# Kernel optimization log

Hardware: AMD Instinct MI355X
Metric: run time of the kernel (lower is better)

Reference implementation:

```python
import jax, jax.numpy as jnp
import numpy as np

N_FFT = 4096
HOP = 1024
WIN = 300          # wiener_win_len (frames per independent Wiener chunk)
EPS = 1e-10
SCALE_FACTOR = 10.0


def hann(n):
    # torch.hann_window (periodic)
    return 0.5 * (1.0 - jnp.cos(2.0 * jnp.pi * jnp.arange(n) / n))


def stft(x, window):
    # x: (N, C, T) -> complex (N, C, B, F), center=True, reflect pad, onesided
    pad = N_FFT // 2
    xp = jnp.pad(x, ((0, 0), (0, 0), (pad, pad)), mode='reflect')
    n_frames = 1 + (xp.shape[-1] - N_FFT) // HOP
    idx = jnp.arange(n_frames)[:, None] * HOP + jnp.arange(N_FFT)[None, :]
    frames = xp[..., idx] * window                      # (N,C,F,n_fft)
    spec = jnp.fft.rfft(frames, axis=-1)                # (N,C,F,B)
    return jnp.swapaxes(spec, -1, -2)                   # (N,C,B,F)


def istft(spec, window, length):
    # spec: (..., B, F) complex -> (..., length) real; center=True inverse
    frames = jnp.fft.irfft(jnp.swapaxes(spec, -1, -2), n=N_FFT, axis=-1) * window
    n_frames = frames.shape[-2]
    out_len = N_FFT + HOP * (n_frames - 1)
    idx = jnp.arange(n_frames)[:, None] * HOP + jnp.arange(N_FFT)[None, :]
    out = jnp.zeros(frames.shape[:-2] + (out_len,), frames.dtype).at[..., idx].add(frames)
    wsum = jnp.zeros((out_len,), frames.dtype).at[idx].add(
        jnp.broadcast_to(window ** 2, idx.shape))
    out = out / jnp.where(wsum > 1e-11, wsum, 1.0)
    pad = N_FFT // 2
    return out[..., pad:pad + length]


def wiener_chunk(v, x, niter):
    # openunmix.filtering.wiener (softmask=False, residual=False) on one chunk.
    # v: (T, B, C, S) real target magnitudes; x: (T, B, C) complex mix STFT.
    phase = jnp.exp(1j * jnp.angle(x))                  # mixture phase init
    y = (v * phase[..., None]).astype(jnp.complex64)    # (T,B,C,S)
    max_abs = jnp.maximum(1.0, jnp.max(jnp.abs(x)) / SCALE_FACTOR)
    x = x / max_abs
    y = y / max_abs
    C = x.shape[-1]
    reg = np.sqrt(EPS) * jnp.eye(C, dtype=jnp.complex64)
    for _ in range(niter):  # expectation_maximization, one pass per iter
        psd = jnp.mean(jnp.abs(y) ** 2, axis=2)         # (T,B,S) channel-avg PSD
        # spatial covariance per bin/source, normalized by eps + sum_t psd
        R = jnp.einsum('tbcs,tbds->bcds', y, jnp.conj(y))
        R = R / (EPS + jnp.sum(psd, axis=0))[:, None, None, :]
        Cxx = reg + jnp.einsum('tbs,bcds->tbcd', psd.astype(jnp.complex64), R)
        inv = jnp.linalg.inv(Cxx)                       # (T,B,C,C)
        gain = jnp.einsum('bacs,tbcd->tbads', R, inv) * psd[:, :, None, None, :]
        y = jnp.einsum('tbacs,tbc->tbas', gain, x)      # (T,B,C,S)
    return y * max_abs


def setup_inputs() -> dict:
    key = jax.random.key(0)
    k1, k2 = jax.random.split(key)
    audio = jax.random.normal(k1, (2, 2, 613376), dtype=jnp.float32)
    W = jax.random.normal(k2, (4, 2049), dtype=jnp.float32)  # per-target per-bin mask logits
    return {'audio': audio, 'W': W, 'niter': 1}


def reference(audio, W, niter):
    window = hann(N_FFT).astype(audio.dtype)
    mix = stft(audio, window)                           # (N,C,B,F) complex
    X = jnp.abs(mix)                                    # ComplexNorm power=1
    # target models (stand-in: per-bin sigmoid masks); input detached as in torch
    Xd = jax.lax.stop_gradient(X)
    masks = jax.nn.sigmoid(W)                           # (S,B)
    specs = Xd[..., None] * jnp.transpose(masks)[None, None, :, None, :]  # (N,C,B,F,S)
    v = jnp.transpose(specs, (0, 3, 2, 1, 4))           # (N,F,B,C,S)
    xm = jnp.transpose(mix, (0, 3, 2, 1))               # (N,F,B,C)
    N, F, B, C = xm.shape
    S = v.shape[-1]
    n_chunks = F // WIN
    vc = v.reshape(N, n_chunks, WIN, B, C, S)
    xc = xm.reshape(N, n_chunks, WIN, B, C)
    wfun = lambda vv, xx: wiener_chunk(vv, xx, niter)
    yc = jax.vmap(jax.vmap(wfun))(vc, xc)               # (N,chunks,T,B,C,S)
    y = yc.reshape(N, F, B, C, S)
    y = jnp.transpose(y, (0, 4, 3, 2, 1))               # (N,S,C,B,F)
    estimates = istft(y, window, audio.shape[-1])       # (N,S,C,T)
    return estimates
```

## Files before the change

### kernel.cpp

```cpp
#include <hip/hip_runtime.h>
#include <math.h>

#define TLEN 613376
#define OLEN 617472
#define NFR  600
#define NB   2049
#define PI_F  3.14159265358979323846f
#define PI2_F 6.28318530717958647693f
#define PHYS(i) ((i) + ((i) >> 4))

__device__ __forceinline__ float winf(int j) {
  return 0.5f - 0.5f * __cosf(1.5339807878856412e-3f * (float)j);
}

__device__ __forceinline__ float wsum_at(int m) {
  int f_max = m >> 10; if (f_max > 599) f_max = 599;
  int f_min = (m - 3072) >> 10; if (f_min < 0) f_min = 0;
  float ws = 0.f;
  for (int f2 = f_min; f2 <= f_max; ++f2) {
    float w = winf(m - (f2 << 10));
    ws += w * w;
  }
  return (ws > 1e-11f) ? ws : 1.0f;
}

__device__ __forceinline__ float reflect_load(const float* __restrict__ x, int pos) {
  int k = pos - 2048;
  if (k < 0) k = -k;
  else if (k >= TLEN) k = 2 * TLEN - 2 - k;
  return x[k];
}

__device__ __forceinline__ float2 cmul(float2 a, float2 b) {
  return make_float2(a.x * b.x - a.y * b.y, a.x * b.y + a.y * b.x);
}
__device__ __forceinline__ float2 cadd(float2 a, float2 b) { return make_float2(a.x + b.x, a.y + b.y); }
__device__ __forceinline__ float2 csub(float2 a, float2 b) { return make_float2(a.x - b.x, a.y - b.y); }
template<int SGN>
__device__ __forceinline__ float2 muli(float2 a) {
  return (SGN > 0) ? make_float2(-a.y, a.x) : make_float2(a.y, -a.x);
}

template<int SGN>
__device__ __forceinline__ void fft4(float2 v[4]) {
  float2 t0 = cadd(v[0], v[2]), t1 = csub(v[0], v[2]);
  float2 t2 = cadd(v[1], v[3]), t3 = csub(v[1], v[3]);
  float2 it3 = muli<SGN>(t3);
  v[0] = cadd(t0, t2); v[2] = csub(t0, t2);
  v[1] = cadd(t1, it3); v[3] = csub(t1, it3);
}

template<int SGN>
__device__ __forceinline__ void fft8(float2 v[8]) {
  const float C = 0.70710678118654752440f;
  const float s = (SGN > 0) ? 1.0f : -1.0f;
  float2 t0 = cadd(v[0], v[4]), t1 = csub(v[0], v[4]);
  float2 t2 = cadd(v[2], v[6]), t3 = csub(v[2], v[6]);
  float2 e0 = cadd(t0, t2), e2 = csub(t0, t2);
  float2 it3 = muli<SGN>(t3);
  float2 e1 = cadd(t1, it3), e3 = csub(t1, it3);
  t0 = cadd(v[1], v[5]); t1 = csub(v[1], v[5]);
  t2 = cadd(v[3], v[7]); t3 = csub(v[3], v[7]);
  float2 o0 = cadd(t0, t2), o2 = csub(t0, t2);
  it3 = muli<SGN>(t3);
  float2 o1 = cadd(t1, it3), o3 = csub(t1, it3);
  float2 o1w = make_float2(C * (o1.x - s * o1.y), C * (o1.y + s * o1.x));
  float2 o2w = muli<SGN>(o2);
  float2 o3w = make_float2(C * (-o3.x - s * o3.y), C * (-o3.y + s * o3.x));
  v[0] = cadd(e0, o0);  v[4] = csub(e0, o0);
  v[1] = cadd(e1, o1w); v[5] = csub(e1, o1w);
  v[2] = cadd(e2, o2w); v[6] = csub(e2, o2w);
  v[3] = cadd(e3, o3w); v[7] = csub(e3, o3w);
}

template<int SGN>
__device__ __forceinline__ void twiddle8(float2 v[8], float ang) {
  float sn, cs;
  __sincosf((SGN > 0) ? ang : -ang, &sn, &cs);
  float2 w1 = make_float2(cs, sn);
  float2 w = w1;
  v[1] = cmul(v[1], w);
#pragma unroll
  for (int r = 2; r < 8; ++r) { w = cmul(w, w1); v[r] = cmul(v[r], w); }
}

template<int SGN>
__device__ __forceinline__ void fft2048_mid(float2* lds, float2 v[8], int tid) {
  fft8<SGN>(v);
#pragma unroll
  for (int r = 0; r < 8; ++r) { int i = tid * 8 + r; lds[PHYS(i)] = v[r]; }
  __syncthreads();
#pragma unroll
  for (int r = 0; r < 8; ++r) v[r] = lds[PHYS(tid + 256 * r)];
  twiddle8<SGN>(v, PI2_F * (1.0f / 64.0f) * (float)(tid & 7));
  fft8<SGN>(v);
  __syncthreads();
#pragma unroll
  for (int r = 0; r < 8; ++r) { int i = ((tid >> 3) << 6) + (tid & 7) + 8 * r; lds[PHYS(i)] = v[r]; }
  __syncthreads();
#pragma unroll
  for (int r = 0; r < 8; ++r) v[r] = lds[PHYS(tid + 256 * r)];
  twiddle8<SGN>(v, PI2_F * (1.0f / 512.0f) * (float)(tid & 63));
  fft8<SGN>(v);
  __syncthreads();
#pragma unroll
  for (int r = 0; r < 8; ++r) { int i = ((tid >> 6) << 9) + (tid & 63) + 64 * r; lds[PHYS(i)] = v[r]; }
  __syncthreads();
}

template<int SGN>
__device__ __forceinline__ void fft2048_last(const float2* lds, int jj, float2 u[4]) {
#pragma unroll
  for (int r = 0; r < 4; ++r) u[r] = lds[PHYS(jj + 512 * r)];
  float sn, cs;
  float ang = PI2_F * (1.0f / 2048.0f) * (float)jj;
  __sincosf((SGN > 0) ? ang : -ang, &sn, &cs);
  float2 w1 = make_float2(cs, sn);
  float2 w2 = cmul(w1, w1);
  float2 w3 = cmul(w2, w1);
  u[1] = cmul(u[1], w1); u[2] = cmul(u[2], w2); u[3] = cmul(u[3], w3);
  fft4<SGN>(u);
}

__global__ __launch_bounds__(256, 6) void stft_kernel(const float* __restrict__ audio,
                                                      float2* __restrict__ X) {
  __shared__ float2 lds[2176];
  int bid = blockIdx.x;
  int f  = bid % NFR;
  int nc = bid / NFR;
  const float* x = audio + (size_t)nc * TLEN;
  int tid = threadIdx.x;
  int base = f * 1024;
  float2 v[8];
#pragma unroll
  for (int r = 0; r < 8; ++r) {
    int k = tid + 256 * r;
    int j0 = 2 * k;
    v[r] = make_float2(reflect_load(x, base + j0)     * winf(j0),
                       reflect_load(x, base + j0 + 1) * winf(j0 + 1));
  }
  fft2048_mid<-1>(lds, v, tid);
  fft2048_last<-1>(lds, tid,        v);
  fft2048_last<-1>(lds, tid + 256,  v + 4);
  __syncthreads();
#pragma unroll
  for (int r = 0; r < 4; ++r) lds[PHYS(tid + 512 * r)] = v[r];
#pragma unroll
  for (int r = 0; r < 4; ++r) lds[PHYS(tid + 256 + 512 * r)] = v[4 + r];
  __syncthreads();
  float2* out = X + (size_t)bid * NB;
  float sn0, cs0;
  __sincosf(-PI_F * (float)tid * (1.0f / 2048.0f), &sn0, &cs0);
  float2 ph = make_float2(cs0, sn0);
  const float2 rot = make_float2(0.92387953251128675613f, -0.38268343236508977173f);
#pragma unroll
  for (int r = 0; r < 9; ++r) {
    int k = tid + 256 * r;
    if (k <= 2048) {
      float2 Zk = lds[PHYS(k & 2047)];
      float2 Zm = lds[PHYS((2048 - k) & 2047)];
      float Ex = 0.5f * (Zk.x + Zm.x), Ey = 0.5f * (Zk.y - Zm.y);
      float Dx = 0.5f * (Zk.x - Zm.x), Dy = 0.5f * (Zk.y + Zm.y);
      float Ox = Dy, Oy = -Dx;
      out[k] = make_float2(Ex + Ox * ph.x - Oy * ph.y, Ey + Ox * ph.y + Oy * ph.x);
    }
    ph = cmul(ph, rot);
  }
}

__global__ __launch_bounds__(256) void stats_kernel(const float2* __restrict__ X,
                                                    float* __restrict__ stats4,
                                                    unsigned int* __restrict__ maxsq) {
  __shared__ unsigned int sm;
  if (threadIdx.x == 0) sm = 0u;
  __syncthreads();
  int b = blockIdx.x * 256 + threadIdx.x;
  bool ok = (b < NB);
  int g = blockIdx.y;
  int n = g >> 1, chunk = g & 1;
  int t0 = blockIdx.z * 75;
  const float2* X0 = X + ((size_t)(n * 2 + 0) * NFR + chunk * 300 + t0) * NB + (ok ? b : 0);
  const float2* X1 = X + ((size_t)(n * 2 + 1) * NFR + chunk * 300 + t0) * NB + (ok ? b : 0);
  float s00 = 0.f, s11 = 0.f, sre = 0.f, sim = 0.f, lmax = 0.f;
  if (ok) {
    for (int t = 0; t < 75; ++t) {
      float2 a = X0[(size_t)t * NB];
      float2 c = X1[(size_t)t * NB];
      float pa = a.x * a.x + a.y * a.y;
      float pc = c.x * c.x + c.y * c.y;
      s00 += pa; s11 += pc;
      sre += a.x * c.x + a.y * c.y;
      sim += a.y * c.x - a.x * c.y;
      lmax = fmaxf(lmax, fmaxf(pa, pc));
    }
  }
  atomicMax(&sm, __float_as_uint(lmax));
  __syncthreads();
  if (threadIdx.x == 0) atomicMax(&maxsq[g], sm);
  if (ok) {
    float* sp = stats4 + ((size_t)g * NB + b) * 4;
    unsafeAtomicAdd(sp + 0, s00);
    unsafeAtomicAdd(sp + 1, s11);
    unsafeAtomicAdd(sp + 2, sre);
    unsafeAtomicAdd(sp + 3, sim);
  }
}

__global__ __launch_bounds__(256) void alpha_kernel(const float* __restrict__ Wmask,
                                                    const float4* __restrict__ stats4,
                                                    const unsigned int* __restrict__ maxsq,
                                                    float* __restrict__ alpha,
                                                    float* __restrict__ Ksum) {
  int idx = blockIdx.x * 256 + threadIdx.x;
  if (idx >= 4 * NB) return;
  int b = idx % NB;
  int g = idx / NB;
  float ma2 = fmaxf(1.0f, __uint_as_float(maxsq[g]) * 0.01f);
  float4 s4 = stats4[(size_t)g * NB + b];
  float P = 0.5f * (s4.x + s4.y) / ma2;
  float K = 0.f;
#pragma unroll
  for (int s = 0; s < 4; ++s) {
    float mv = 1.0f / (1.0f + expf(-Wmask[s * NB + b]));
    float m2 = mv * mv;
    float a = (m2 * m2) / (1e-10f + m2 * P);
    alpha[(size_t)(g * 4 + s) * NB + b] = a;
    K += a;
  }
  Ksum[(size_t)g * NB + b] = K;
}

__global__ __launch_bounds__(256) void wiener_kernel(const float2* __restrict__ X,
                                                     const float4* __restrict__ stats4,
                                                     const float* __restrict__ Ksum,
                                                     const unsigned int* __restrict__ maxsq,
                                                     float2* __restrict__ Wc) {
  int idx = blockIdx.x * 256 + threadIdx.x;
  if (idx >= 4 * 300 * NB) return;
  int b = idx % NB;
  int gt = idx / NB;
  int t = gt % 300;
  int g = gt / 300;
  int n = g >> 1, chunk = g & 1;
  int f = chunk * 300 + t;
  float ima2 = 1.0f / fmaxf(1.0f, __uint_as_float(maxsq[g]) * 0.01f);
  float4 s4 = stats4[(size_t)g * NB + b];
  float g00 = s4.x * ima2, g11 = s4.y * ima2, gre = s4.z * ima2, gim = s4.w * ima2;
  float K = Ksum[(size_t)g * NB + b];
  float2 x0 = X[((size_t)(n * 2 + 0) * NFR + f) * NB + b];
  float2 x1 = X[((size_t)(n * 2 + 1) * NFR + f) * NB + b];
  float ph = 0.5f * ((x0.x * x0.x + x0.y * x0.y) + (x1.x * x1.x + x1.y * x1.y)) * ima2;
  float pk = ph * K;
  float M00 = 1e-5f + pk * g00;
  float M11 = 1e-5f + pk * g11;
  float Mre = pk * gre, Mim = pk * gim;
  float det = M00 * M11 - (Mre * Mre + Mim * Mim);
  float sc = ph / det;
  float u0x = M11 * x0.x - (Mre * x1.x - Mim * x1.y);
  float u0y = M11 * x0.y - (Mre * x1.y + Mim * x1.x);
  float u1x = M00 * x1.x - (Mre * x0.x + Mim * x0.y);
  float u1y = M00 * x1.y - (Mre * x0.y - Mim * x0.x);
  float w0x = g00 * u0x + (gre * u1x - gim * u1y);
  float w0y = g00 * u0y + (gre * u1y + gim * u1x);
  float w1x = (gre * u0x + gim * u0y) + g11 * u1x;
  float w1y = (gre * u0y - gim * u0x) + g11 * u1y;
  float2* out = Wc + ((size_t)(n * NFR + f) * 2) * NB + b;
  out[0]  = make_float2(w0x * sc, w0y * sc);
  out[NB] = make_float2(w1x * sc, w1y * sc);
}

template<int MODE>
__global__ __launch_bounds__(256, 6) void istft_pass_kernel(const float2* __restrict__ Wc,
                                                            const float* __restrict__ alpha,
                                                            float* __restrict__ accum,
                                                            float* __restrict__ out,
                                                            int pass) {
  __shared__ float2 lds[2176];
  int bid = blockIdx.x;
  int fi = bid % 150;
  int plane = bid / 150;
  int c = plane & 1;
  int s = (plane >> 1) & 3;
  int n = plane >> 3;
  int f = 4 * fi + pass;
  int g = n * 2 + (f >= 300 ? 1 : 0);
  int tid = threadIdx.x;
  const float2* Wrow = Wc + ((size_t)(n * NFR + f) * 2 + c) * NB;
  const float*  arow = alpha + (size_t)(g * 4 + s) * NB;
  float* acc = accum + (size_t)plane * OLEN + (size_t)f * 1024;

  float2 pre[8];
  if (MODE >= 1) {
#pragma unroll
    for (int half = 0; half < 2; ++half) {
#pragma unroll
      for (int r = 0; r < 4; ++r) {
        int m = tid + 256 * half + 512 * r;
        pre[half * 4 + r] = *(const float2*)&acc[2 * m];
      }
    }
  }

  float2 v[8];
  float sn0, cs0;
  __sincosf(PI_F * (float)tid * (1.0f / 2048.0f), &sn0, &cs0);
  float2 ph = make_float2(cs0, sn0);
  const float2 rot = make_float2(0.92387953251128675613f, 0.38268343236508977173f);
#pragma unroll
  for (int r = 0; r < 8; ++r) {
    int k = tid + 256 * r;
    float ak = arow[k];
    float2 sk = Wrow[k]; sk.x *= ak; sk.y *= ak;
    int rk = 2048 - k;
    float am = arow[rk];
    float2 sv = Wrow[rk]; sv.x *= am; sv.y *= am;
    float Ex = 0.5f * (sk.x + sv.x), Ey = 0.5f * (sk.y - sv.y);
    float Dx = 0.5f * (sk.x - sv.x), Dy = 0.5f * (sk.y + sv.y);
    float Ox = Dx * ph.x - Dy * ph.y, Oy = Dx * ph.y + Dy * ph.x;
    v[r] = make_float2(Ex - Oy, Ey + Ox);
    ph = cmul(ph, rot);
  }
  fft2048_mid<1>(lds, v, tid);
  float* outp = out + (size_t)plane * TLEN;
  const float scale = 1.0f / 2048.0f;
#pragma unroll
  for (int half = 0; half < 2; ++half) {
    int jj = tid + 256 * half;
    float2 u[4];
    fft2048_last<1>(lds, jj, u);
#pragma unroll
    for (int r = 0; r < 4; ++r) {
      int m = jj + 512 * r;
      int j0 = 2 * m;
      float2 val = make_float2(u[r].x * scale * winf(j0),
                               u[r].y * scale * winf(j0 + 1));
      float2* p = (float2*)&acc[j0];
      if (MODE == 0) {
        *p = val;
      } else if (MODE == 1) {
        float2 o = pre[half * 4 + r];
        val.x += o.x; val.y += o.y;
        *p = val;
      } else {
        int gm = f * 1024 + j0;
        if (gm < 615424) {
          float2 o = pre[half * 4 + r];
          val.x += o.x; val.y += o.y;
          float i0, i1;
          if (gm >= 3072 && gm + 1 < 614400) {
            i0 = 0.66666666666666667f; i1 = i0;
          } else {
            i0 = 1.0f / wsum_at(gm); i1 = 1.0f / wsum_at(gm + 1);
          }
          float2* po = (float2*)&outp[gm - 2048];
          *po = make_float2(val.x * i0, val.y * i1);
        }
      }
    }
  }
  if (MODE == 0 && fi == 149) {
    float* tail = accum + (size_t)plane * OLEN + 614400;
    for (int i = tid; i < OLEN - 614400; i += 256) tail[i] = 0.f;
  }
  if (MODE == 2 && fi == 0) {
    float* accp = accum + (size_t)plane * OLEN;
    for (int m = 2048 + tid; m < 3072; m += 256) {
      outp[m - 2048] = accp[m] / wsum_at(m);
    }
  }
}

extern "C" void kernel_launch(void* const* d_in, const int* in_sizes, int n_in,
                              void* d_out, int out_size, void* d_ws, size_t ws_size,
                              hipStream_t stream) {
  const float* audio = (const float*)d_in[0];
  const float* Wmask = (const float*)d_in[1];
  float* out = (float*)d_out;

  char* ws = (char*)d_ws;
  const size_t off_stats4 = 0;
  const size_t off_maxsq  = 131136;
  const size_t zero_span  = 131200;
  const size_t off_X      = zero_span;
  const size_t off_Wc     = off_X + 39340800;
  const size_t off_accum  = off_Wc + 39340800;
  const size_t off_alpha  = off_accum + 39518208;
  const size_t off_Ksum   = off_alpha + 131136;

  float*        stats4f = (float*)(ws + off_stats4);
  float4*       stats4  = (float4*)(ws + off_stats4);
  unsigned int* maxsq   = (unsigned int*)(ws + off_maxsq);
  float2*       X       = (float2*)(ws + off_X);
  float2*       Wc      = (float2*)(ws + off_Wc);
  float*        accum   = (float*)(ws + off_accum);
  float*        alpha   = (float*)(ws + off_alpha);
  float*        Ksum    = (float*)(ws + off_Ksum);

  hipMemsetAsync(ws, 0, zero_span, stream);

  stft_kernel<<<2400, 256, 0, stream>>>(audio, X);
  stats_kernel<<<dim3(9, 4, 4), 256, 0, stream>>>(X, stats4f, maxsq);
  alpha_kernel<<<(4 * NB + 255) / 256, 256, 0, stream>>>(Wmask, stats4, maxsq, alpha, Ksum);
  wiener_kernel<<<(4 * 300 * NB + 255) / 256, 256, 0, stream>>>(X, stats4, Ksum, maxsq, Wc);
  istft_pass_kernel<0><<<2400, 256, 0, stream>>>(Wc, alpha, accum, out, 0);
  istft_pass_kernel<1><<<2400, 256, 0, stream>>>(Wc, alpha, accum, out, 1);
  istft_pass_kernel<1><<<2400, 256, 0, stream>>>(Wc, alpha, accum, out, 2);
  istft_pass_kernel<2><<<2400, 256, 0, stream>>>(Wc, alpha, accum, out, 3);
}
```

Before: 204.6 us.

## Fuse four iSTFT passes into one kernel with register overlap-add and combine pass

Replaces four sequential iSTFT launches, which read-modify-wrote a full-length accumulation buffer, with a single kernel in which each block transforms four consecutive frames and overlap-adds them in registers. Each block writes its interior samples straight to the output and stores its head and tail partial sums to a scratch buffer. A small combine kernel then adds neighbouring partials and applies the constant window normalisation. This cuts launches and global accumulator traffic, and reuses the X workspace region for the partials. In exchange it holds more live registers (occupancy hint lowered to 4) and adds one extra launch.

After: 345.8 us. 1.69x slower.

```diff
diff --git a/kernel.cpp b/kernel.cpp
--- a/kernel.cpp
+++ b/kernel.cpp
@@ -2,7 +2,6 @@
 #include <math.h>
 
 #define TLEN 613376
-#define OLEN 617472
 #define NFR  600
 #define NB   2049
 #define PI_F  3.14159265358979323846f
@@ -269,104 +268,134 @@
   out[NB] = make_float2(w1x * sc, w1y * sc);
 }
 
-template<int MODE>
-__global__ __launch_bounds__(256, 6) void istft_pass_kernel(const float2* __restrict__ Wc,
-                                                            const float* __restrict__ alpha,
-                                                            float* __restrict__ accum,
-                                                            float* __restrict__ out,
-                                                            int pass) {
+__global__ __launch_bounds__(256, 4) void istft_fused_kernel(const float2* __restrict__ Wc,
+                                                             const float* __restrict__ alpha,
+                                                             float* __restrict__ part,
+                                                             float* __restrict__ out) {
   __shared__ float2 lds[2176];
   int bid = blockIdx.x;
-  int fi = bid % 150;
+  int j = bid % 150;
   int plane = bid / 150;
   int c = plane & 1;
   int s = (plane >> 1) & 3;
   int n = plane >> 3;
-  int f = 4 * fi + pass;
-  int g = n * 2 + (f >= 300 ? 1 : 0);
+  int f0 = 4 * j;
+  int g = n * 2 + (j >= 75 ? 1 : 0);
   int tid = threadIdx.x;
-  const float2* Wrow = Wc + ((size_t)(n * NFR + f) * 2 + c) * NB;
-  const float*  arow = alpha + (size_t)(g * 4 + s) * NB;
-  float* acc = accum + (size_t)plane * OLEN + (size_t)f * 1024;
-
-  float2 pre[8];
-  if (MODE >= 1) {
-#pragma unroll
-    for (int half = 0; half < 2; ++half) {
-#pragma unroll
-      for (int r = 0; r < 4; ++r) {
-        int m = tid + 256 * half + 512 * r;
-        pre[half * 4 + r] = *(const float2*)&acc[2 * m];
-      }
-    }
-  }
-
-  float2 v[8];
+  const float* __restrict__ arow = alpha + (size_t)(g * 4 + s) * NB;
+  float* __restrict__ outp = out + (size_t)plane * TLEN;
+  float* __restrict__ ppart = part + ((size_t)plane * 150 + j) * 2 * 3072;
+
+  const float scale = 1.0f / 2048.0f;
+  float w0[8], w1[8];
+#pragma unroll
+  for (int k = 0; k < 8; ++k) {
+    int j0 = 2 * tid + 512 * k;
+    w0[k] = winf(j0) * scale;
+    w1[k] = winf(j0 + 1) * scale;
+  }
   float sn0, cs0;
   __sincosf(PI_F * (float)tid * (1.0f / 2048.0f), &sn0, &cs0);
-  float2 ph = make_float2(cs0, sn0);
+  const float2 ph0 = make_float2(cs0, sn0);
   const float2 rot = make_float2(0.92387953251128675613f, 0.38268343236508977173f);
-#pragma unroll
-  for (int r = 0; r < 8; ++r) {
-    int k = tid + 256 * r;
-    float ak = arow[k];
-    float2 sk = Wrow[k]; sk.x *= ak; sk.y *= ak;
-    int rk = 2048 - k;
-    float am = arow[rk];
-    float2 sv = Wrow[rk]; sv.x *= am; sv.y *= am;
-    float Ex = 0.5f * (sk.x + sv.x), Ey = 0.5f * (sk.y - sv.y);
-    float Dx = 0.5f * (sk.x - sv.x), Dy = 0.5f * (sk.y + sv.y);
-    float Ox = Dx * ph.x - Dy * ph.y, Oy = Dx * ph.y + Dy * ph.x;
-    v[r] = make_float2(Ex - Oy, Ey + Ox);
-    ph = cmul(ph, rot);
-  }
-  fft2048_mid<1>(lds, v, tid);
-  float* outp = out + (size_t)plane * TLEN;
-  const float scale = 1.0f / 2048.0f;
-#pragma unroll
-  for (int half = 0; half < 2; ++half) {
-    int jj = tid + 256 * half;
-    float2 u[4];
-    fft2048_last<1>(lds, jj, u);
-#pragma unroll
-    for (int r = 0; r < 4; ++r) {
-      int m = jj + 512 * r;
-      int j0 = 2 * m;
-      float2 val = make_float2(u[r].x * scale * winf(j0),
-                               u[r].y * scale * winf(j0 + 1));
-      float2* p = (float2*)&acc[j0];
-      if (MODE == 0) {
-        *p = val;
-      } else if (MODE == 1) {
-        float2 o = pre[half * 4 + r];
-        val.x += o.x; val.y += o.y;
-        *p = val;
-      } else {
-        int gm = f * 1024 + j0;
-        if (gm < 615424) {
-          float2 o = pre[half * 4 + r];
-          val.x += o.x; val.y += o.y;
-          float i0, i1;
-          if (gm >= 3072 && gm + 1 < 614400) {
-            i0 = 0.66666666666666667f; i1 = i0;
-          } else {
-            i0 = 1.0f / wsum_at(gm); i1 = 1.0f / wsum_at(gm + 1);
-          }
-          float2* po = (float2*)&outp[gm - 2048];
-          *po = make_float2(val.x * i0, val.y * i1);
-        }
+
+  float2 acc[14];
+#pragma unroll
+  for (int q = 0; q < 14; ++q) acc[q] = make_float2(0.f, 0.f);
+
+#pragma unroll 4
+  for (int d = 0; d < 4; ++d) {
+    const float2* __restrict__ Wrow = Wc + ((size_t)(n * NFR + (f0 + d)) * 2 + c) * NB;
+    float2 v[8];
+    float2 ph = ph0;
+#pragma unroll
+    for (int r = 0; r < 8; ++r) {
+      int k = tid + 256 * r;
+      float akv = arow[k];
+      float amv = arow[2048 - k];
+      float2 sk = Wrow[k];        sk.x *= akv; sk.y *= akv;
+      float2 sv = Wrow[2048 - k]; sv.x *= amv; sv.y *= amv;
+      float Ex = 0.5f * (sk.x + sv.x), Ey = 0.5f * (sk.y - sv.y);
+      float Dx = 0.5f * (sk.x - sv.x), Dy = 0.5f * (sk.y + sv.y);
+      float Ox = Dx * ph.x - Dy * ph.y, Oy = Dx * ph.y + Dy * ph.x;
+      v[r] = make_float2(Ex - Oy, Ey + Ox);
+      ph = cmul(ph, rot);
+    }
+    fft2048_mid<1>(lds, v, tid);
+#pragma unroll
+    for (int half = 0; half < 2; ++half) {
+      int jj = tid + 256 * half;
+      float2 u[4];
+      fft2048_last<1>(lds, jj, u);
+#pragma unroll
+      for (int r = 0; r < 4; ++r) {
+        int k = half + 2 * r;
+        acc[k + 2 * d].x += u[r].x * w0[k];
+        acc[k + 2 * d].y += u[r].y * w1[k];
       }
     }
-  }
-  if (MODE == 0 && fi == 149) {
-    float* tail = accum + (size_t)plane * OLEN + 614400;
-    for (int i = tid; i < OLEN - 614400; i += 256) tail[i] = 0.f;
-  }
-  if (MODE == 2 && fi == 0) {
-    float* accp = accum + (size_t)plane * OLEN;
-    for (int m = 2048 + tid; m < 3072; m += 256) {
-      outp[m - 2048] = accp[m] / wsum_at(m);
-    }
+    __syncthreads();
+  }
+
+  int base2 = 2 * tid;
+  const float inv15 = 0.66666666666666667f;
+
+  {
+    int p = 4096 * j + base2 + 512 * 6 - 2048;
+    *(float2*)&outp[p]       = make_float2(acc[6].x * inv15, acc[6].y * inv15);
+    *(float2*)&outp[p + 512] = make_float2(acc[7].x * inv15, acc[7].y * inv15);
+  }
+  if (j == 0) {
+#pragma unroll
+    for (int q = 4; q <= 5; ++q) {
+      int p = base2 + 512 * q;
+      outp[p - 2048] = acc[q].x / wsum_at(p);
+      outp[p - 2047] = acc[q].y / wsum_at(p + 1);
+    }
+  } else {
+#pragma unroll
+    for (int q = 0; q < 6; ++q) {
+      int idx = base2 + 512 * q;
+      *(float2*)&ppart[idx] = acc[q];
+    }
+  }
+  if (j == 149) {
+#pragma unroll
+    for (int q = 8; q <= 9; ++q) {
+      int p = 4096 * 149 + base2 + 512 * q;
+      outp[p - 2048] = acc[q].x / wsum_at(p);
+      outp[p - 2047] = acc[q].y / wsum_at(p + 1);
+    }
+  } else {
+#pragma unroll
+    for (int q = 8; q < 14; ++q) {
+      int idx = base2 + 512 * (q - 8);
+      *(float2*)&ppart[3072 + idx] = acc[q];
+    }
+  }
+}
+
+__global__ __launch_bounds__(256) void combine_kernel(const float* __restrict__ part,
+                                                      float* __restrict__ out) {
+  int bid = blockIdx.x;
+  int jm = bid % 149;
+  int plane = bid / 149;
+  int j = jm + 1;
+  const float4* hp = (const float4*)(part + (((size_t)plane * 150 + j) * 2 + 0) * 3072);
+  const float4* tp = (const float4*)(part + (((size_t)plane * 150 + (j - 1)) * 2 + 1) * 3072);
+  float4* outp = (float4*)(out + (size_t)plane * TLEN + (4096 * j - 2048));
+  const float inv15 = 0.66666666666666667f;
+  int t = threadIdx.x;
+#pragma unroll
+  for (int i = 0; i < 3; ++i) {
+    int idx = t + 256 * i;
+    float4 h = hp[idx], tl = tp[idx];
+    float4 o;
+    o.x = (h.x + tl.x) * inv15;
+    o.y = (h.y + tl.y) * inv15;
+    o.z = (h.z + tl.z) * inv15;
+    o.w = (h.w + tl.w) * inv15;
+    outp[idx] = o;
   }
 }
 
@@ -381,20 +410,20 @@
   const size_t off_stats4 = 0;
   const size_t off_maxsq  = 131136;
   const size_t zero_span  = 131200;
-  const size_t off_X      = zero_span;
-  const size_t off_Wc     = off_X + 39340800;
-  const size_t off_accum  = off_Wc + 39340800;
-  const size_t off_alpha  = off_accum + 39518208;
+  const size_t off_alpha  = zero_span;
   const size_t off_Ksum   = off_alpha + 131136;
+  const size_t off_Wc     = off_Ksum + 32784;
+  const size_t off_X      = off_Wc + 39340800;
+  const size_t off_part   = off_X;
 
   float*        stats4f = (float*)(ws + off_stats4);
   float4*       stats4  = (float4*)(ws + off_stats4);
   unsigned int* maxsq   = (unsigned int*)(ws + off_maxsq);
-  float2*       X       = (float2*)(ws + off_X);
-  float2*       Wc      = (float2*)(ws + off_Wc);
-  float*        accum   = (float*)(ws + off_accum);
   float*        alpha   = (float*)(ws + off_alpha);
   float*        Ksum    = (float*)(ws + off_Ksum);
+  float2*       Wc      = (float2*)(ws + off_Wc);
+  float2*       X       = (float2*)(ws + off_X);
+  float*        part    = (float*)(ws + off_part);
 
   hipMemsetAsync(ws, 0, zero_span, stream);
 
@@ -402,8 +431,6 @@
   stats_kernel<<<dim3(9, 4, 4), 256, 0, stream>>>(X, stats4f, maxsq);
   alpha_kernel<<<(4 * NB + 255) / 256, 256, 0, stream>>>(Wmask, stats4, maxsq, alpha, Ksum);
   wiener_kernel<<<(4 * 300 * NB + 255) / 256, 256, 0, stream>>>(X, stats4, Ksum, maxsq, Wc);
-  istft_pass_kernel<0><<<2400, 256, 0, stream>>>(Wc, alpha, accum, out, 0);
-  istft_pass_kernel<1><<<2400, 256, 0, stream>>>(Wc, alpha, accum, out, 1);
-  istft_pass_kernel<1><<<2400, 256, 0, stream>>>(Wc, alpha, accum, out, 2);
-  istft_pass_kernel<2><<<2400, 256, 0, stream>>>(Wc, alpha, accum, out, 3);
-}
+  istft_fused_kernel<<<2400, 256, 0, stream>>>(Wc, alpha, part, out);
+  combine_kernel<<<16 * 149, 256, 0, stream>>>(part, out);
+}
```
